# Kernel tuning notes

Hardware: AMD Instinct MI355X
Metric: run time of the kernel (lower is better)

The kernel has to match this reference:

```python
import jax, jax.numpy as jnp
import numpy as np

N = 50000
E = 800000
IN_C, C1, C2 = 256, 128, 64
BN_EPS = 1e-5


def setup_inputs() -> dict:
    key = jax.random.key(0)
    ks = jax.random.split(key, 12)
    x = jax.random.normal(ks[0], (N, IN_C), dtype=jnp.float32)
    edge_index = jax.random.randint(ks[1], (2, E), 0, N, dtype=jnp.int32)
    edge_weight = jax.random.uniform(ks[2], (E,), dtype=jnp.float32)
    W1 = jax.random.normal(ks[3], (IN_C, C1), dtype=jnp.float32) * 0.05
    b1 = jnp.zeros((C1,), dtype=jnp.float32)
    W2 = jax.random.normal(ks[4], (C1, C2), dtype=jnp.float32) * 0.05
    b2 = jnp.zeros((C2,), dtype=jnp.float32)
    g1 = jnp.ones((C1,), dtype=jnp.float32)
    be1 = jnp.zeros((C1,), dtype=jnp.float32)
    g2 = jnp.ones((C2,), dtype=jnp.float32)
    be2 = jnp.zeros((C2,), dtype=jnp.float32)
    Ws = jax.random.normal(ks[5], (IN_C, C2), dtype=jnp.float32) * 0.05
    bs = jnp.zeros((C2,), dtype=jnp.float32)
    return dict(x=x, edge_index=edge_index, edge_weight=edge_weight,
                W1=W1, b1=b1, W2=W2, b2=b2, g1=g1, be1=be1, g2=g2, be2=be2,
                Ws=Ws, bs=bs)


def _gcn_conv(h_in, row, col, ew, W, b):
    # PyG GCNConv: transform then symmetric-normalized aggregation with self-loops
    n = h_in.shape[0]
    h = h_in @ W  # [N, C]
    loop = jnp.arange(n, dtype=row.dtype)
    row_f = jnp.concatenate([row, loop])
    col_f = jnp.concatenate([col, loop])
    ew_f = jnp.concatenate([ew, jnp.ones((n,), dtype=ew.dtype)])
    deg = jax.ops.segment_sum(ew_f, col_f, num_segments=n)  # degree at targets
    dinv = jnp.where(deg > 0, jax.lax.rsqrt(deg), 0.0)
    norm = dinv[row_f] * ew_f * dinv[col_f]  # [E+N]
    out = jax.ops.segment_sum(h[row_f] * norm[:, None], col_f, num_segments=n)
    return out + b


def _batchnorm(x, gamma, beta):
    mu = jnp.mean(x, axis=0)
    var = jnp.mean(jnp.square(x - mu), axis=0)  # biased, as torch BN forward
    return (x - mu) * jax.lax.rsqrt(var + BN_EPS) * gamma + beta


def reference(x, edge_index, edge_weight, W1, b1, W2, b2, g1, be1, g2, be2, Ws, bs):
    row, col = edge_index[0], edge_index[1]
    skip = x @ Ws + bs
    x1 = _gcn_conv(x, row, col, edge_weight, W1, b1)
    x1 = jax.nn.gelu(_batchnorm(x1, g1, be1), approximate=False)
    # dropout is identity in deterministic/eval reference
    x2 = _gcn_conv(x1, row, col, edge_weight, W2, b2)
    x2 = _batchnorm(x2, g2, be2) + skip
    return x2
```

## Files before the change

kernel.cpp:

```cpp
#include <hip/hip_runtime.h>
#include <math.h>

constexpr int NN = 50000;
constexpr int EE = 800000;
constexpr int INC = 256, CC1 = 128, CC2 = 64;

typedef short bf16x8 __attribute__((ext_vector_type(8)));
typedef float f32x4 __attribute__((ext_vector_type(4)));

__device__ __forceinline__ unsigned short f2bf(float f) {
    unsigned int u = __builtin_bit_cast(unsigned int, f);
    u = (u + 0x7FFFu + ((u >> 16) & 1u)) >> 16;
    return (unsigned short)u;
}
__device__ __forceinline__ float bf2f(unsigned short u) {
    return __builtin_bit_cast(float, (unsigned int)u << 16);
}
__device__ __forceinline__ float bflo(unsigned int w) {
    return __builtin_bit_cast(float, w << 16);
}
__device__ __forceinline__ float bfhi(unsigned int w) {
    return __builtin_bit_cast(float, w & 0xFFFF0000u);
}
__device__ __forceinline__ unsigned int packbf2(float lo, float hi) {
    return (unsigned int)f2bf(lo) | ((unsigned int)f2bf(hi) << 16);
}

__global__ void __launch_bounds__(256) gemm1_rank_kernel(
        const float* __restrict__ A, const float* __restrict__ B1, const float* __restrict__ B2,
        unsigned short* __restrict__ C1, unsigned short* __restrict__ C2,
        const int* __restrict__ col, const float* __restrict__ ew,
        unsigned long long* __restrict__ packed, int* __restrict__ rank, int gemm_blocks) {
    constexpr int K = INC, N1 = CC1, N2 = CC2, NT = N1 + N2;
    constexpr int NG = 64, KC = K / 8, PITCH = K + 8;
    __shared__ unsigned short Blds[NG * PITCH];

    if ((int)blockIdx.x >= gemm_blocks) {
        int e = (blockIdx.x - gemm_blocks) * 256 + threadIdx.x;
        if (e < EE) {
            int c = col[e];
            unsigned int fx = __float2uint_rn(ew[e] * 16777216.0f);
            unsigned long long old =
                atomicAdd(&packed[c], (1ULL << 32) | (unsigned long long)fx);
            rank[e] = (int)(old >> 32);
        }
        return;
    }

    const int tid = threadIdx.x;
    const int wave = tid >> 6, lane = tid & 63;
    const int quad = lane >> 4, nIdx = lane & 15;
    const int row0 = blockIdx.x * 64 + wave * 16;
    const int arow = row0 + nIdx;
    const int arow_c = (arow < NN) ? arow : (NN - 1);

    bf16x8 afrag[K / 32];
    {
        const float* ap = A + (long long)arow_c * K + quad * 8;
#pragma unroll
        for (int s = 0; s < K / 32; s++) {
            float4 lo = *(const float4*)(ap + s * 32);
            float4 hi = *(const float4*)(ap + s * 32 + 4);
            bf16x8 f;
            f[0] = (short)f2bf(lo.x); f[1] = (short)f2bf(lo.y);
            f[2] = (short)f2bf(lo.z); f[3] = (short)f2bf(lo.w);
            f[4] = (short)f2bf(hi.x); f[5] = (short)f2bf(hi.y);
            f[6] = (short)f2bf(hi.z); f[7] = (short)f2bf(hi.w);
            afrag[s] = f;
        }
    }

    for (int g0 = 0; g0 < NT; g0 += NG) {
        if (g0) __syncthreads();
        {
            int n = tid & 63;
            int gcol = g0 + n;
            const float* Bp = B1; int Nw = N1; int bcol = gcol;
            if (gcol >= N1) { Bp = B2; Nw = N2; bcol = gcol - N1; }
            for (int kc = tid >> 6; kc < KC; kc += 4) {
                int k0 = kc * 8;
                bf16x8 v;
#pragma unroll
                for (int j = 0; j < 8; j++)
                    v[j] = (short)f2bf(Bp[(long long)(k0 + j) * Nw + bcol]);
                *(bf16x8*)(&Blds[n * PITCH + k0]) = v;
            }
        }
        __syncthreads();
#pragma unroll
        for (int t = 0; t < NG / 16; t++) {
            const unsigned short* bp = &Blds[(t * 16 + nIdx) * PITCH + quad * 8];
            f32x4 acc = {0.0f, 0.0f, 0.0f, 0.0f};
#pragma unroll
            for (int s = 0; s < K / 32; s++) {
                bf16x8 bf = *(const bf16x8*)(bp + s * 32);
                acc = __builtin_amdgcn_mfma_f32_16x16x32_bf16(afrag[s], bf, acc, 0, 0, 0);
            }
            int ocol = g0 + t * 16 + nIdx;
#pragma unroll
            for (int r = 0; r < 4; r++) {
                int orow = row0 + quad * 4 + r;
                if (orow < NN) {
                    if (ocol < N1)
                        C1[(long long)orow * N1 + ocol] = f2bf(acc[r]);
                    else
                        C2[(long long)orow * N2 + (ocol - N1)] = f2bf(acc[r]);
                }
            }
        }
    }
}


__global__ void alloc_kernel(const unsigned long long* __restrict__ packed,
                             float* __restrict__ dinv, int* __restrict__ start,
                             int* __restrict__ count, int* __restrict__ cursor, int n) {
    int i = blockIdx.x * 256 + threadIdx.x;
    if (i < n) {
        unsigned long long p = packed[i];
        int cnt = (int)(p >> 32);
        float deg = 1.0f + (float)(unsigned int)(p & 0xFFFFFFFFu) * (1.0f / 16777216.0f);
        dinv[i] = rsqrtf(deg);
        count[i] = cnt;
        start[i] = atomicAdd(cursor, cnt);
    }
}

__global__ void fill_kernel(const int* __restrict__ row, const int* __restrict__ col,
                            const float* __restrict__ ew, const float* __restrict__ dinv,
                            const int* __restrict__ rank, const int* __restrict__ start,
                            int2* __restrict__ pairs, int e_cnt) {
    int e = blockIdx.x * 256 + threadIdx.x;
    if (e < e_cnt) {
        int r = row[e], c = col[e];
        float nv = dinv[r] * ew[e] * dinv[c];
        int pos = start[c] + rank[e];
        pairs[pos] = make_int2(r, __float_as_int(nv));
    }
}

__global__ void __launch_bounds__(256) gemm2_kernel(
        const unsigned short* __restrict__ A, const float* __restrict__ B,
        unsigned short* __restrict__ C,
        const float* __restrict__ sum, const float* __restrict__ sumsq,
        const float* __restrict__ gamma, const float* __restrict__ beta, int n_rows) {
    constexpr int K = CC1, N = CC2;
    constexpr int KC = K / 8, PITCH = K + 8;
    __shared__ unsigned short Blds[N * PITCH];
    __shared__ float scL[K], shL[K];

    const int tid = threadIdx.x;
    if (tid < K) {
        float inv_n = 1.0f / (float)n_rows;
        float mu = sum[tid] * inv_n;
        float var = fmaxf(sumsq[tid] * inv_n - mu * mu, 0.0f);
        float sc = gamma[tid] * rsqrtf(var + 1e-5f);
        scL[tid] = sc; shL[tid] = beta[tid] - mu * sc;
    }
    {
        int n = tid & 63;
        for (int kc = tid >> 6; kc < KC; kc += 4) {
            int k0 = kc * 8;
            bf16x8 v;
#pragma unroll
            for (int j = 0; j < 8; j++)
                v[j] = (short)f2bf(B[(long long)(k0 + j) * N + n]);
            *(bf16x8*)(&Blds[n * PITCH + k0]) = v;
        }
    }
    __syncthreads();

    const int wave = tid >> 6, lane = tid & 63;
    const int quad = lane >> 4, nIdx = lane & 15;
    const int row0 = blockIdx.x * 64 + wave * 16;
    const int arow = row0 + nIdx;
    const int arow_c = (arow < n_rows) ? arow : (n_rows - 1);

    bf16x8 afrag[K / 32];
    {
        const unsigned short* ap = A + (long long)arow_c * K + quad * 8;
#pragma unroll
        for (int s = 0; s < K / 32; s++) {
            bf16x8 raw = *(const bf16x8*)(ap + s * 32);
            int kb = s * 32 + quad * 8;
            bf16x8 f;
#pragma unroll
            for (int j = 0; j < 8; j++) {
                float u = bf2f((unsigned short)raw[j]) * scL[kb + j] + shL[kb + j];
                float v = u * 0.5f * (1.0f + erff(u * 0.70710678f));
                f[j] = (short)f2bf(v);
            }
            afrag[s] = f;
        }
    }
#pragma unroll
    for (int t = 0; t < N / 16; t++) {
        const unsigned short* bp = &Blds[(t * 16 + nIdx) * PITCH + quad * 8];
        f32x4 acc = {0.0f, 0.0f, 0.0f, 0.0f};
#pragma unroll
        for (int s = 0; s < K / 32; s++) {
            bf16x8 bf = *(const bf16x8*)(bp + s * 32);
            acc = __builtin_amdgcn_mfma_f32_16x16x32_bf16(afrag[s], bf, acc, 0, 0, 0);
        }
        int ocol = t * 16 + nIdx;
#pragma unroll
        for (int r = 0; r < 4; r++) {
            int orow = row0 + quad * 4 + r;
            if (orow < n_rows)
                C[(long long)orow * N + ocol] = f2bf(acc[r]);
        }
    }
}

template<int C>
__global__ void gather_agg(const unsigned short* __restrict__ h, const float* __restrict__ dinv,
                           const float* __restrict__ b, const int2* __restrict__ pairs,
                           const int* __restrict__ start, const int* __restrict__ count,
                           unsigned short* __restrict__ outb, int n) {
    constexpr int TPN = C / 8;
    int gid = blockIdx.x * 256 + threadIdx.x;
    int node = gid / TPN;
    int part = gid - node * TPN;
    if (node >= n) return;
    int c8 = part * 8;
    float d = dinv[node];
    float d2 = d * d;
    uint4 hv = *(const uint4*)(h + (long long)node * C + c8);
    float a0 = bflo(hv.x) * d2 + b[c8 + 0];
    float a1 = bfhi(hv.x) * d2 + b[c8 + 1];
    float a2 = bflo(hv.y) * d2 + b[c8 + 2];
    float a3 = bfhi(hv.y) * d2 + b[c8 + 3];
    float a4 = bflo(hv.z) * d2 + b[c8 + 4];
    float a5 = bfhi(hv.z) * d2 + b[c8 + 5];
    float a6 = bflo(hv.w) * d2 + b[c8 + 6];
    float a7 = bfhi(hv.w) * d2 + b[c8 + 7];
    const int2* pp = pairs + start[node];
    int m = count[node];
    int j = 0;
    for (; j + 8 <= m; j += 8) {
        int2 p[8];
#pragma unroll
        for (int i = 0; i < 8; i++) p[i] = pp[j + i];
        uint4 v[8];
#pragma unroll
        for (int i = 0; i < 8; i++)
            v[i] = *(const uint4*)(h + (long long)p[i].x * C + c8);
#pragma unroll
        for (int i = 0; i < 8; i++) {
            float w = __int_as_float(p[i].y);
            a0 += bflo(v[i].x) * w; a1 += bfhi(v[i].x) * w;
            a2 += bflo(v[i].y) * w; a3 += bfhi(v[i].y) * w;
            a4 += bflo(v[i].z) * w; a5 += bfhi(v[i].z) * w;
            a6 += bflo(v[i].w) * w; a7 += bfhi(v[i].w) * w;
        }
    }
    for (; j < m; j++) {
        int2 p = pp[j];
        float w = __int_as_float(p.y);
        uint4 v = *(const uint4*)(h + (long long)p.x * C + c8);
        a0 += bflo(v.x) * w; a1 += bfhi(v.x) * w;
        a2 += bflo(v.y) * w; a3 += bfhi(v.y) * w;
        a4 += bflo(v.z) * w; a5 += bfhi(v.z) * w;
        a6 += bflo(v.w) * w; a7 += bfhi(v.w) * w;
    }
    uint4 o;
    o.x = packbf2(a0, a1); o.y = packbf2(a2, a3);
    o.z = packbf2(a4, a5); o.w = packbf2(a6, a7);
    *(uint4*)(outb + (long long)node * C + c8) = o;
}

template<int C>
__global__ void bnstats_bf16(const unsigned short* __restrict__ x, float* __restrict__ sum,
                             float* __restrict__ sumsq, int n) {
    constexpr int PR = C / 2;
    constexpr int RG = 256 / PR;
    constexpr int ROWS = 256;
    const int cp = threadIdx.x % PR;
    const int rg = threadIdx.x / PR;
    const int base = blockIdx.x * ROWS;
    const unsigned int* xu = (const unsigned int*)x;
    float s0 = 0, ss0 = 0, s1 = 0, ss1 = 0;
    for (int r = rg; r < ROWS; r += RG) {
        int nn = base + r;
        if (nn < n) {
            unsigned int v = xu[(long long)nn * PR + cp];
            float lo = bflo(v), hi = bfhi(v);
            s0 += lo; ss0 += lo * lo; s1 += hi; ss1 += hi * hi;
        }
    }
    __shared__ float red[4][256];
    red[0][threadIdx.x] = s0; red[1][threadIdx.x] = ss0;
    red[2][threadIdx.x] = s1; red[3][threadIdx.x] = ss1;
    __syncthreads();
    if (rg == 0) {
#pragma unroll
        for (int g = 1; g < RG; g++) {
            s0 += red[0][g * PR + cp]; ss0 += red[1][g * PR + cp];
            s1 += red[2][g * PR + cp]; ss1 += red[3][g * PR + cp];
        }
        atomicAdd(&sum[2 * cp], s0);     atomicAdd(&sumsq[2 * cp], ss0);
        atomicAdd(&sum[2 * cp + 1], s1); atomicAdd(&sumsq[2 * cp + 1], ss1);
    }
}

__global__ void final_kernel(const unsigned short* __restrict__ agg2b,
                             const unsigned short* __restrict__ skipb,
                             const float* __restrict__ sum, const float* __restrict__ sumsq,
                             const float* __restrict__ gamma, const float* __restrict__ beta,
                             const float* __restrict__ bs, float* __restrict__ out, int n) {
    __shared__ float sc[CC2], sh[CC2];
    if (threadIdx.x < CC2) {
        float inv_n = 1.0f / (float)n;
        float mu = sum[threadIdx.x] * inv_n;
        float var = fmaxf(sumsq[threadIdx.x] * inv_n - mu * mu, 0.0f);
        float s = gamma[threadIdx.x] * rsqrtf(var + 1e-5f);
        sc[threadIdx.x] = s;
        sh[threadIdx.x] = beta[threadIdx.x] - mu * s + bs[threadIdx.x];
    }
    __syncthreads();
    int i2 = blockIdx.x * 256 + threadIdx.x;
    if (i2 >= n * (CC2 / 2)) return;
    unsigned int av = ((const unsigned int*)agg2b)[i2];
    unsigned int sv = ((const unsigned int*)skipb)[i2];
    int c2 = (i2 % (CC2 / 2)) * 2;
    float2 o;
    o.x = bflo(av) * sc[c2] + sh[c2] + bflo(sv);
    o.y = bfhi(av) * sc[c2 + 1] + sh[c2 + 1] + bfhi(sv);
    *(float2*)(out + 2 * (long long)i2) = o;
}


extern "C" void kernel_launch(void* const* d_in, const int* in_sizes, int n_in,
                              void* d_out, int out_size, void* d_ws, size_t ws_size,
                              hipStream_t stream) {
    const float* x   = (const float*)d_in[0];
    const int*   ei  = (const int*)d_in[1];
    const float* ew  = (const float*)d_in[2];
    const float* W1  = (const float*)d_in[3];
    const float* b1  = (const float*)d_in[4];
    const float* W2  = (const float*)d_in[5];
    const float* b2  = (const float*)d_in[6];
    const float* g1  = (const float*)d_in[7];
    const float* be1 = (const float*)d_in[8];
    const float* g2  = (const float*)d_in[9];
    const float* be2 = (const float*)d_in[10];
    const float* Ws  = (const float*)d_in[11];
    const float* bs  = (const float*)d_in[12];
    float* out = (float*)d_out;

    const int* row = ei;
    const int* col = ei + EE;

    char* wp = (char*)d_ws;
    float* stats = (float*)wp;
    float* sum1   = stats;
    float* sumsq1 = stats + 128;
    float* sum2   = stats + 256;
    float* sumsq2 = stats + 320;
    int*   cursor = (int*)(wp + 4096);
    unsigned long long* packed = (unsigned long long*)(wp + 4112);
    char* p2 = wp + 4112 + (size_t)NN * 8;
    int*   rank   = (int*)p2;             p2 += (size_t)EE * 4;
    int*   startp = (int*)p2;             p2 += (size_t)NN * 4;
    int*   countp = (int*)p2;             p2 += (size_t)NN * 4;
    float* dinv   = (float*)p2;           p2 += (size_t)NN * 4;
    int2*  pairs  = (int2*)p2;            p2 += (size_t)EE * 8;
    unsigned short* h1b   = (unsigned short*)p2; p2 += (size_t)NN * CC1 * 2;
    unsigned short* h2b   = (unsigned short*)p2; p2 += (size_t)NN * CC2 * 2;
    unsigned short* agg1b = (unsigned short*)p2; p2 += (size_t)NN * CC1 * 2;
    unsigned short* agg2b = (unsigned short*)p2; p2 += (size_t)NN * CC2 * 2;
    unsigned short* skipb = (unsigned short*)p2; p2 += (size_t)NN * CC2 * 2;

    const int nb_N = (NN + 255) / 256;
    const int nb_E = (EE + 255) / 256;
    const int nb_G = (NN + 63) / 64;

    hipMemsetAsync(wp, 0, 4112 + (size_t)NN * 8, stream);

    gemm1_rank_kernel<<<nb_G + nb_E, 256, 0, stream>>>(
        x, W1, Ws, h1b, skipb, col, ew, packed, rank, nb_G);

    alloc_kernel<<<nb_N, 256, 0, stream>>>(packed, dinv, startp, countp, cursor, NN);
    fill_kernel<<<nb_E, 256, 0, stream>>>(row, col, ew, dinv, rank, startp, pairs, EE);

    gather_agg<CC1><<<(NN * (CC1 / 8) + 255) / 256, 256, 0, stream>>>(
        h1b, dinv, b1, pairs, startp, countp, agg1b, NN);
    bnstats_bf16<CC1><<<(NN + 255) / 256, 256, 0, stream>>>(agg1b, sum1, sumsq1, NN);

    gemm2_kernel<<<nb_G, 256, 0, stream>>>(agg1b, W2, h2b, sum1, sumsq1, g1, be1, NN);
    gather_agg<CC2><<<(NN * (CC2 / 8) + 255) / 256, 256, 0, stream>>>(
        h2b, dinv, b2, pairs, startp, countp, agg2b, NN);
    bnstats_bf16<CC2><<<(NN + 255) / 256, 256, 0, stream>>>(agg2b, sum2, sumsq2, NN);

    final_kernel<<<(NN * (CC2 / 2) + 255) / 256, 256, 0, stream>>>(
        agg2b, skipb, sum2, sumsq2, g2, be2, bs, out, NN);

    (void)in_sizes; (void)n_in; (void)out_size; (void)ws_size;
}
```

Measured before the change: 317.6 us.

## Fuse all GCN stages into one persistent cooperative kernel with grid syncs

Replaces the memset and the chain of separate kernel launches with a single cooperative persistent kernel. Stages are separated by grid.sync and use grid-stride loops. BN statistics for layer 1 are computed inside the gather stage through block reductions plus atomics, which removes a separate stats pass over agg1. This removes launch overhead and some memory re-reads, at the cost of grid-wide barriers, an occupancy-limited grid, and a GEMM1 that no longer overlaps with the rank atomics.

Result: slower. 755.3 us (+137.8%).

```diff
diff --git a/kernel.cpp b/kernel.cpp
--- a/kernel.cpp
+++ b/kernel.cpp
@@ -1,9 +1,19 @@
 #include <hip/hip_runtime.h>
+#include <hip/hip_cooperative_groups.h>
 #include <math.h>
+
+namespace cg = cooperative_groups;
 
 constexpr int NN = 50000;
 constexpr int EE = 800000;
 constexpr int INC = 256, CC1 = 128, CC2 = 64;
+
+constexpr int T1    = (NN + 63) / 64;
+constexpr int CE    = EE / 256;
+constexpr int CNODE = (NN + 255) / 256;
+constexpr int J1    = NN * (CC1 / 8) / 256;
+constexpr int J2    = (NN * (CC2 / 8) + 255) / 256;
+constexpr int F2    = NN * (CC2 / 2) / 256;
 
 typedef short bf16x8 __attribute__((ext_vector_type(8)));
 typedef float f32x4 __attribute__((ext_vector_type(4)));
@@ -26,374 +36,443 @@
     return (unsigned int)f2bf(lo) | ((unsigned int)f2bf(hi) << 16);
 }
 
-__global__ void __launch_bounds__(256) gemm1_rank_kernel(
-        const float* __restrict__ A, const float* __restrict__ B1, const float* __restrict__ B2,
-        unsigned short* __restrict__ C1, unsigned short* __restrict__ C2,
-        const int* __restrict__ col, const float* __restrict__ ew,
-        unsigned long long* __restrict__ packed, int* __restrict__ rank, int gemm_blocks) {
-    constexpr int K = INC, N1 = CC1, N2 = CC2, NT = N1 + N2;
-    constexpr int NG = 64, KC = K / 8, PITCH = K + 8;
-    __shared__ unsigned short Blds[NG * PITCH];
-
-    if ((int)blockIdx.x >= gemm_blocks) {
-        int e = (blockIdx.x - gemm_blocks) * 256 + threadIdx.x;
-        if (e < EE) {
-            int c = col[e];
-            unsigned int fx = __float2uint_rn(ew[e] * 16777216.0f);
-            unsigned long long old =
-                atomicAdd(&packed[c], (1ULL << 32) | (unsigned long long)fx);
-            rank[e] = (int)(old >> 32);
-        }
-        return;
-    }
-
+struct Params {
+    const float *x, *ew, *W1, *b1, *W2, *b2, *g1, *be1, *g2, *be2, *Ws, *bs;
+    const int *row, *col;
+    float* out;
+    float* stats;
+    int* cursor;
+    unsigned long long* packed;
+    int* rank;
+    int* startp;
+    int* countp;
+    float* dinv;
+    int2* pairs;
+    unsigned short *h1b, *h2b, *agg1b, *agg2b, *skipb;
+};
+
+union SharedU {
+    unsigned short b1[64 * (INC + 8)];
+    struct {
+        unsigned short b2[64 * (CC1 + 8)];
+        float sc[CC1], sh[CC1];
+    } g2;
+    float red[2048];
+    struct { float sc[CC2], sh[CC2]; } fin;
+};
+
+__global__ void __launch_bounds__(256, 4) mega_kernel(Params P) {
+    cg::grid_group grid = cg::this_grid();
     const int tid = threadIdx.x;
+    const int bid = blockIdx.x;
+    const int G = gridDim.x;
     const int wave = tid >> 6, lane = tid & 63;
     const int quad = lane >> 4, nIdx = lane & 15;
-    const int row0 = blockIdx.x * 64 + wave * 16;
-    const int arow = row0 + nIdx;
-    const int arow_c = (arow < NN) ? arow : (NN - 1);
-
-    bf16x8 afrag[K / 32];
+
+    __shared__ SharedU sh;
+
+    for (int c = bid; c < CNODE; c += G) {
+        int i = c * 256 + tid;
+        if (i < NN) P.packed[i] = 0ULL;
+    }
+    if (bid == 0) {
+        for (int i = tid; i < 384; i += 256) P.stats[i] = 0.0f;
+        if (tid == 0) *P.cursor = 0;
+    }
+    grid.sync();
+
     {
-        const float* ap = A + (long long)arow_c * K + quad * 8;
-#pragma unroll
-        for (int s = 0; s < K / 32; s++) {
-            float4 lo = *(const float4*)(ap + s * 32);
-            float4 hi = *(const float4*)(ap + s * 32 + 4);
-            bf16x8 f;
-            f[0] = (short)f2bf(lo.x); f[1] = (short)f2bf(lo.y);
-            f[2] = (short)f2bf(lo.z); f[3] = (short)f2bf(lo.w);
-            f[4] = (short)f2bf(hi.x); f[5] = (short)f2bf(hi.y);
-            f[6] = (short)f2bf(hi.z); f[7] = (short)f2bf(hi.w);
-            afrag[s] = f;
-        }
-    }
-
-    for (int g0 = 0; g0 < NT; g0 += NG) {
-        if (g0) __syncthreads();
+        constexpr int K = INC, N1 = CC1, N2 = CC2, NT = N1 + N2;
+        constexpr int KC = K / 8, PITCH = K + 8;
+        for (int t = bid; t < T1; t += G) {
+            const int row0 = t * 64 + wave * 16;
+            const int arow = row0 + nIdx;
+            const int arow_c = (arow < NN) ? arow : (NN - 1);
+            bf16x8 afrag[K / 32];
+            {
+                const float* ap = P.x + (long long)arow_c * K + quad * 8;
+#pragma unroll
+                for (int s = 0; s < K / 32; s++) {
+                    float4 lo = *(const float4*)(ap + s * 32);
+                    float4 hi = *(const float4*)(ap + s * 32 + 4);
+                    bf16x8 f;
+                    f[0] = (short)f2bf(lo.x); f[1] = (short)f2bf(lo.y);
+                    f[2] = (short)f2bf(lo.z); f[3] = (short)f2bf(lo.w);
+                    f[4] = (short)f2bf(hi.x); f[5] = (short)f2bf(hi.y);
+                    f[6] = (short)f2bf(hi.z); f[7] = (short)f2bf(hi.w);
+                    afrag[s] = f;
+                }
+            }
+            for (int g0 = 0; g0 < NT; g0 += 64) {
+                __syncthreads();
+                {
+                    int n = tid & 63;
+                    int gcol = g0 + n;
+                    const float* Bp = P.W1; int Nw = N1; int bcol = gcol;
+                    if (gcol >= N1) { Bp = P.Ws; Nw = N2; bcol = gcol - N1; }
+                    for (int kc = tid >> 6; kc < KC; kc += 4) {
+                        int k0 = kc * 8;
+                        bf16x8 v;
+#pragma unroll
+                        for (int j = 0; j < 8; j++)
+                            v[j] = (short)f2bf(Bp[(long long)(k0 + j) * Nw + bcol]);
+                        *(bf16x8*)(&sh.b1[n * PITCH + k0]) = v;
+                    }
+                }
+                __syncthreads();
+#pragma unroll
+                for (int t4 = 0; t4 < 4; t4++) {
+                    const unsigned short* bp = &sh.b1[(t4 * 16 + nIdx) * PITCH + quad * 8];
+                    f32x4 acc = {0.0f, 0.0f, 0.0f, 0.0f};
+#pragma unroll
+                    for (int s = 0; s < K / 32; s++) {
+                        bf16x8 bf = *(const bf16x8*)(bp + s * 32);
+                        acc = __builtin_amdgcn_mfma_f32_16x16x32_bf16(afrag[s], bf, acc, 0, 0, 0);
+                    }
+                    int ocol = g0 + t4 * 16 + nIdx;
+#pragma unroll
+                    for (int r = 0; r < 4; r++) {
+                        int orow = row0 + quad * 4 + r;
+                        if (orow < NN) {
+                            if (ocol < N1)
+                                P.h1b[(long long)orow * N1 + ocol] = f2bf(acc[r]);
+                            else
+                                P.skipb[(long long)orow * N2 + (ocol - N1)] = f2bf(acc[r]);
+                        }
+                    }
+                }
+            }
+        }
+        for (int c = bid; c < CE; c += G) {
+            int e = c * 256 + tid;
+            int cc = P.col[e];
+            unsigned int fx = __float2uint_rn(P.ew[e] * 16777216.0f);
+            unsigned long long old =
+                atomicAdd(&P.packed[cc], (1ULL << 32) | (unsigned long long)fx);
+            P.rank[e] = (int)(old >> 32);
+        }
+    }
+    grid.sync();
+
+    for (int c = bid; c < CNODE; c += G) {
+        int i = c * 256 + tid;
+        if (i < NN) {
+            unsigned long long p = P.packed[i];
+            int cnt = (int)(p >> 32);
+            float deg = 1.0f + (float)(unsigned int)(p & 0xFFFFFFFFu) * (1.0f / 16777216.0f);
+            P.dinv[i] = rsqrtf(deg);
+            P.countp[i] = cnt;
+            P.startp[i] = atomicAdd(P.cursor, cnt);
+        }
+    }
+    grid.sync();
+
+    for (int c = bid; c < CE; c += G) {
+        int e = c * 256 + tid;
+        int r = P.row[e], cc = P.col[e];
+        float nv = P.dinv[r] * P.ew[e] * P.dinv[cc];
+        P.pairs[P.startp[cc] + P.rank[e]] = make_int2(r, __float_as_int(nv));
+    }
+    grid.sync();
+
+    {
+        const int part = tid & 15;
+        const int c8 = part * 8;
+        float s[8] = {0,0,0,0,0,0,0,0}, ssq[8] = {0,0,0,0,0,0,0,0};
+        for (int j = bid; j < J1; j += G) {
+            int node = (j * 256 + tid) >> 4;
+            float d = P.dinv[node];
+            float d2 = d * d;
+            uint4 hv = *(const uint4*)(P.h1b + (long long)node * CC1 + c8);
+            float a0 = bflo(hv.x) * d2 + P.b1[c8 + 0];
+            float a1 = bfhi(hv.x) * d2 + P.b1[c8 + 1];
+            float a2 = bflo(hv.y) * d2 + P.b1[c8 + 2];
+            float a3 = bfhi(hv.y) * d2 + P.b1[c8 + 3];
+            float a4 = bflo(hv.z) * d2 + P.b1[c8 + 4];
+            float a5 = bfhi(hv.z) * d2 + P.b1[c8 + 5];
+            float a6 = bflo(hv.w) * d2 + P.b1[c8 + 6];
+            float a7 = bfhi(hv.w) * d2 + P.b1[c8 + 7];
+            const int2* pp = P.pairs + P.startp[node];
+            int m = P.countp[node];
+            int jj = 0;
+            for (; jj + 8 <= m; jj += 8) {
+                int2 p[8];
+#pragma unroll
+                for (int i = 0; i < 8; i++) p[i] = pp[jj + i];
+                uint4 v[8];
+#pragma unroll
+                for (int i = 0; i < 8; i++)
+                    v[i] = *(const uint4*)(P.h1b + (long long)p[i].x * CC1 + c8);
+#pragma unroll
+                for (int i = 0; i < 8; i++) {
+                    float w = __int_as_float(p[i].y);
+                    a0 += bflo(v[i].x) * w; a1 += bfhi(v[i].x) * w;
+                    a2 += bflo(v[i].y) * w; a3 += bfhi(v[i].y) * w;
+                    a4 += bflo(v[i].z) * w; a5 += bfhi(v[i].z) * w;
+                    a6 += bflo(v[i].w) * w; a7 += bfhi(v[i].w) * w;
+                }
+            }
+            for (; jj < m; jj++) {
+                int2 p = pp[jj];
+                float w = __int_as_float(p.y);
+                uint4 v = *(const uint4*)(P.h1b + (long long)p.x * CC1 + c8);
+                a0 += bflo(v.x) * w; a1 += bfhi(v.x) * w;
+                a2 += bflo(v.y) * w; a3 += bfhi(v.y) * w;
+                a4 += bflo(v.z) * w; a5 += bfhi(v.z) * w;
+                a6 += bflo(v.w) * w; a7 += bfhi(v.w) * w;
+            }
+            uint4 o;
+            o.x = packbf2(a0, a1); o.y = packbf2(a2, a3);
+            o.z = packbf2(a4, a5); o.w = packbf2(a6, a7);
+            *(uint4*)(P.agg1b + (long long)node * CC1 + c8) = o;
+            s[0] += a0; ssq[0] += a0 * a0; s[1] += a1; ssq[1] += a1 * a1;
+            s[2] += a2; ssq[2] += a2 * a2; s[3] += a3; ssq[3] += a3 * a3;
+            s[4] += a4; ssq[4] += a4 * a4; s[5] += a5; ssq[5] += a5 * a5;
+            s[6] += a6; ssq[6] += a6 * a6; s[7] += a7; ssq[7] += a7 * a7;
+        }
+        __syncthreads();
+#pragma unroll
+        for (int k = 0; k < 8; k++) sh.red[tid * 8 + k] = s[k];
+        __syncthreads();
+        if (tid < CC1) {
+            int p = tid >> 3, k = tid & 7;
+            float acc = 0.0f;
+#pragma unroll
+            for (int g = 0; g < 16; g++) acc += sh.red[(g * 16 + p) * 8 + k];
+            atomicAdd(&P.stats[p * 8 + k], acc);
+        }
+        __syncthreads();
+#pragma unroll
+        for (int k = 0; k < 8; k++) sh.red[tid * 8 + k] = ssq[k];
+        __syncthreads();
+        if (tid < CC1) {
+            int p = tid >> 3, k = tid & 7;
+            float acc = 0.0f;
+#pragma unroll
+            for (int g = 0; g < 16; g++) acc += sh.red[(g * 16 + p) * 8 + k];
+            atomicAdd(&P.stats[128 + p * 8 + k], acc);
+        }
+    }
+    grid.sync();
+
+    {
+        constexpr int K = CC1, N = CC2;
+        constexpr int KC = K / 8, PITCH = K + 8;
+        __syncthreads();
+        if (tid < K) {
+            float inv_n = 1.0f / (float)NN;
+            float mu = P.stats[tid] * inv_n;
+            float var = fmaxf(P.stats[128 + tid] * inv_n - mu * mu, 0.0f);
+            float sc = P.g1[tid] * rsqrtf(var + 1e-5f);
+            sh.g2.sc[tid] = sc;
+            sh.g2.sh[tid] = P.be1[tid] - mu * sc;
+        }
         {
             int n = tid & 63;
-            int gcol = g0 + n;
-            const float* Bp = B1; int Nw = N1; int bcol = gcol;
-            if (gcol >= N1) { Bp = B2; Nw = N2; bcol = gcol - N1; }
             for (int kc = tid >> 6; kc < KC; kc += 4) {
                 int k0 = kc * 8;
                 bf16x8 v;
 #pragma unroll
                 for (int j = 0; j < 8; j++)
-                    v[j] = (short)f2bf(Bp[(long long)(k0 + j) * Nw + bcol]);
-                *(bf16x8*)(&Blds[n * PITCH + k0]) = v;
-            }
-        }
-        __syncthreads();
-#pragma unroll
-        for (int t = 0; t < NG / 16; t++) {
-            const unsigned short* bp = &Blds[(t * 16 + nIdx) * PITCH + quad * 8];
-            f32x4 acc = {0.0f, 0.0f, 0.0f, 0.0f};
+                    v[j] = (short)f2bf(P.W2[(long long)(k0 + j) * N + n]);
+                *(bf16x8*)(&sh.g2.b2[n * PITCH + k0]) = v;
+            }
+        }
+        __syncthreads();
+        for (int t = bid; t < T1; t += G) {
+            const int row0 = t * 64 + wave * 16;
+            const int arow = row0 + nIdx;
+            const int arow_c = (arow < NN) ? arow : (NN - 1);
+            bf16x8 afrag[K / 32];
+            const unsigned short* ap = P.agg1b + (long long)arow_c * K + quad * 8;
 #pragma unroll
             for (int s = 0; s < K / 32; s++) {
-                bf16x8 bf = *(const bf16x8*)(bp + s * 32);
-                acc = __builtin_amdgcn_mfma_f32_16x16x32_bf16(afrag[s], bf, acc, 0, 0, 0);
-            }
-            int ocol = g0 + t * 16 + nIdx;
-#pragma unroll
-            for (int r = 0; r < 4; r++) {
-                int orow = row0 + quad * 4 + r;
-                if (orow < NN) {
-                    if (ocol < N1)
-                        C1[(long long)orow * N1 + ocol] = f2bf(acc[r]);
-                    else
-                        C2[(long long)orow * N2 + (ocol - N1)] = f2bf(acc[r]);
-                }
-            }
-        }
-    }
-}
-
-
-__global__ void alloc_kernel(const unsigned long long* __restrict__ packed,
-                             float* __restrict__ dinv, int* __restrict__ start,
-                             int* __restrict__ count, int* __restrict__ cursor, int n) {
-    int i = blockIdx.x * 256 + threadIdx.x;
-    if (i < n) {
-        unsigned long long p = packed[i];
-        int cnt = (int)(p >> 32);
-        float deg = 1.0f + (float)(unsigned int)(p & 0xFFFFFFFFu) * (1.0f / 16777216.0f);
-        dinv[i] = rsqrtf(deg);
-        count[i] = cnt;
-        start[i] = atomicAdd(cursor, cnt);
-    }
-}
-
-__global__ void fill_kernel(const int* __restrict__ row, const int* __restrict__ col,
-                            const float* __restrict__ ew, const float* __restrict__ dinv,
-                            const int* __restrict__ rank, const int* __restrict__ start,
-                            int2* __restrict__ pairs, int e_cnt) {
-    int e = blockIdx.x * 256 + threadIdx.x;
-    if (e < e_cnt) {
-        int r = row[e], c = col[e];
-        float nv = dinv[r] * ew[e] * dinv[c];
-        int pos = start[c] + rank[e];
-        pairs[pos] = make_int2(r, __float_as_int(nv));
-    }
-}
-
-__global__ void __launch_bounds__(256) gemm2_kernel(
-        const unsigned short* __restrict__ A, const float* __restrict__ B,
-        unsigned short* __restrict__ C,
-        const float* __restrict__ sum, const float* __restrict__ sumsq,
-        const float* __restrict__ gamma, const float* __restrict__ beta, int n_rows) {
-    constexpr int K = CC1, N = CC2;
-    constexpr int KC = K / 8, PITCH = K + 8;
-    __shared__ unsigned short Blds[N * PITCH];
-    __shared__ float scL[K], shL[K];
-
-    const int tid = threadIdx.x;
-    if (tid < K) {
-        float inv_n = 1.0f / (float)n_rows;
-        float mu = sum[tid] * inv_n;
-        float var = fmaxf(sumsq[tid] * inv_n - mu * mu, 0.0f);
-        float sc = gamma[tid] * rsqrtf(var + 1e-5f);
-        scL[tid] = sc; shL[tid] = beta[tid] - mu * sc;
-    }
+                bf16x8 raw = *(const bf16x8*)(ap + s * 32);
+                int kb = s * 32 + quad * 8;
+                bf16x8 f;
+#pragma unroll
+                for (int j = 0; j < 8; j++) {
+                    float u = bf2f((unsigned short)raw[j]) * sh.g2.sc[kb + j] + sh.g2.sh[kb + j];
+                    float v = u * 0.5f * (1.0f + erff(u * 0.70710678f));
+                    f[j] = (short)f2bf(v);
+                }
+                afrag[s] = f;
+            }
+#pragma unroll
+            for (int t4 = 0; t4 < N / 16; t4++) {
+                const unsigned short* bp = &sh.g2.b2[(t4 * 16 + nIdx) * PITCH + quad * 8];
+                f32x4 acc = {0.0f, 0.0f, 0.0f, 0.0f};
+#pragma unroll
+                for (int s = 0; s < K / 32; s++) {
+                    bf16x8 bf = *(const bf16x8*)(bp + s * 32);
+                    acc = __builtin_amdgcn_mfma_f32_16x16x32_bf16(afrag[s], bf, acc, 0, 0, 0);
+                }
+                int ocol = t4 * 16 + nIdx;
+#pragma unroll
+                for (int r = 0; r < 4; r++) {
+                    int orow = row0 + quad * 4 + r;
+                    if (orow < NN)
+                        P.h2b[(long long)orow * N + ocol] = f2bf(acc[r]);
+                }
+            }
+        }
+    }
+    grid.sync();
+
     {
-        int n = tid & 63;
-        for (int kc = tid >> 6; kc < KC; kc += 4) {
-            int k0 = kc * 8;
-            bf16x8 v;
-#pragma unroll
-            for (int j = 0; j < 8; j++)
-                v[j] = (short)f2bf(B[(long long)(k0 + j) * N + n]);
-            *(bf16x8*)(&Blds[n * PITCH + k0]) = v;
-        }
-    }
-    __syncthreads();
-
-    const int wave = tid >> 6, lane = tid & 63;
-    const int quad = lane >> 4, nIdx = lane & 15;
-    const int row0 = blockIdx.x * 64 + wave * 16;
-    const int arow = row0 + nIdx;
-    const int arow_c = (arow < n_rows) ? arow : (n_rows - 1);
-
-    bf16x8 afrag[K / 32];
+        const int part = tid & 7;
+        const int c8 = part * 8;
+        float s[8] = {0,0,0,0,0,0,0,0}, ssq[8] = {0,0,0,0,0,0,0,0};
+        for (int j = bid; j < J2; j += G) {
+            int node = (j * 256 + tid) >> 3;
+            if (node < NN) {
+                float d = P.dinv[node];
+                float d2 = d * d;
+                uint4 hv = *(const uint4*)(P.h2b + (long long)node * CC2 + c8);
+                float a0 = bflo(hv.x) * d2 + P.b2[c8 + 0];
+                float a1 = bfhi(hv.x) * d2 + P.b2[c8 + 1];
+                float a2 = bflo(hv.y) * d2 + P.b2[c8 + 2];
+                float a3 = bfhi(hv.y) * d2 + P.b2[c8 + 3];
+                float a4 = bflo(hv.z) * d2 + P.b2[c8 + 4];
+                float a5 = bfhi(hv.z) * d2 + P.b2[c8 + 5];
+                float a6 = bflo(hv.w) * d2 + P.b2[c8 + 6];
+                float a7 = bfhi(hv.w) * d2 + P.b2[c8 + 7];
+                const int2* pp = P.pairs + P.startp[node];
+                int m = P.countp[node];
+                int jj = 0;
+                for (; jj + 8 <= m; jj += 8) {
+                    int2 p[8];
+#pragma unroll
+                    for (int i = 0; i < 8; i++) p[i] = pp[jj + i];
+                    uint4 v[8];
+#pragma unroll
+                    for (int i = 0; i < 8; i++)
+                        v[i] = *(const uint4*)(P.h2b + (long long)p[i].x * CC2 + c8);
+#pragma unroll
+                    for (int i = 0; i < 8; i++) {
+                        float w = __int_as_float(p[i].y);
+                        a0 += bflo(v[i].x) * w; a1 += bfhi(v[i].x) * w;
+                        a2 += bflo(v[i].y) * w; a3 += bfhi(v[i].y) * w;
+                        a4 += bflo(v[i].z) * w; a5 += bfhi(v[i].z) * w;
+                        a6 += bflo(v[i].w) * w; a7 += bfhi(v[i].w) * w;
+                    }
+                }
+                for (; jj < m; jj++) {
+                    int2 p = pp[jj];
+                    float w = __int_as_float(p.y);
+                    uint4 v = *(const uint4*)(P.h2b + (long long)p.x * CC2 + c8);
+                    a0 += bflo(v.x) * w; a1 += bfhi(v.x) * w;
+                    a2 += bflo(v.y) * w; a3 += bfhi(v.y) * w;
+                    a4 += bflo(v.z) * w; a5 += bfhi(v.z) * w;
+                    a6 += bflo(v.w) * w; a7 += bfhi(v.w) * w;
+                }
+                uint4 o;
+                o.x = packbf2(a0, a1); o.y = packbf2(a2, a3);
+                o.z = packbf2(a4, a5); o.w = packbf2(a6, a7);
+                *(uint4*)(P.agg2b + (long long)node * CC2 + c8) = o;
+                s[0] += a0; ssq[0] += a0 * a0; s[1] += a1; ssq[1] += a1 * a1;
+                s[2] += a2; ssq[2] += a2 * a2; s[3] += a3; ssq[3] += a3 * a3;
+                s[4] += a4; ssq[4] += a4 * a4; s[5] += a5; ssq[5] += a5 * a5;
+                s[6] += a6; ssq[6] += a6 * a6; s[7] += a7; ssq[7] += a7 * a7;
+            }
+        }
+        __syncthreads();
+#pragma unroll
+        for (int k = 0; k < 8; k++) sh.red[tid * 8 + k] = s[k];
+        __syncthreads();
+        if (tid < CC2) {
+            int p = tid >> 3, k = tid & 7;
+            float acc = 0.0f;
+#pragma unroll
+            for (int g = 0; g < 32; g++) acc += sh.red[(g * 8 + p) * 8 + k];
+            atomicAdd(&P.stats[256 + p * 8 + k], acc);
+        }
+        __syncthreads();
+#pragma unroll
+        for (int k = 0; k < 8; k++) sh.red[tid * 8 + k] = ssq[k];
+        __syncthreads();
+        if (tid < CC2) {
+            int p = tid >> 3, k = tid & 7;
+            float acc = 0.0f;
+#pragma unroll
+            for (int g = 0; g < 32; g++) acc += sh.red[(g * 8 + p) * 8 + k];
+            atomicAdd(&P.stats[320 + p * 8 + k], acc);
+        }
+    }
+    grid.sync();
+
     {
-        const unsigned short* ap = A + (long long)arow_c * K + quad * 8;
-#pragma unroll
-        for (int s = 0; s < K / 32; s++) {
-            bf16x8 raw = *(const bf16x8*)(ap + s * 32);
-            int kb = s * 32 + quad * 8;
-            bf16x8 f;
-#pragma unroll
-            for (int j = 0; j < 8; j++) {
-                float u = bf2f((unsigned short)raw[j]) * scL[kb + j] + shL[kb + j];
-                float v = u * 0.5f * (1.0f + erff(u * 0.70710678f));
-                f[j] = (short)f2bf(v);
-            }
-            afrag[s] = f;
-        }
-    }
-#pragma unroll
-    for (int t = 0; t < N / 16; t++) {
-        const unsigned short* bp = &Blds[(t * 16 + nIdx) * PITCH + quad * 8];
-        f32x4 acc = {0.0f, 0.0f, 0.0f, 0.0f};
-#pragma unroll
-        for (int s = 0; s < K / 32; s++) {
-            bf16x8 bf = *(const bf16x8*)(bp + s * 32);
-            acc = __builtin_amdgcn_mfma_f32_16x16x32_bf16(afrag[s], bf, acc, 0, 0, 0);
-        }
-        int ocol = t * 16 + nIdx;
-#pragma unroll
-        for (int r = 0; r < 4; r++) {
-            int orow = row0 + quad * 4 + r;
-            if (orow < n_rows)
-                C[(long long)orow * N + ocol] = f2bf(acc[r]);
-        }
-    }
-}
-
-template<int C>
-__global__ void gather_agg(const unsigned short* __restrict__ h, const float* __restrict__ dinv,
-                           const float* __restrict__ b, const int2* __restrict__ pairs,
-                           const int* __restrict__ start, const int* __restrict__ count,
-                           unsigned short* __restrict__ outb, int n) {
-    constexpr int TPN = C / 8;
-    int gid = blockIdx.x * 256 + threadIdx.x;
-    int node = gid / TPN;
-    int part = gid - node * TPN;
-    if (node >= n) return;
-    int c8 = part * 8;
-    float d = dinv[node];
-    float d2 = d * d;
-    uint4 hv = *(const uint4*)(h + (long long)node * C + c8);
-    float a0 = bflo(hv.x) * d2 + b[c8 + 0];
-    float a1 = bfhi(hv.x) * d2 + b[c8 + 1];
-    float a2 = bflo(hv.y) * d2 + b[c8 + 2];
-    float a3 = bfhi(hv.y) * d2 + b[c8 + 3];
-    float a4 = bflo(hv.z) * d2 + b[c8 + 4];
-    float a5 = bfhi(hv.z) * d2 + b[c8 + 5];
-    float a6 = bflo(hv.w) * d2 + b[c8 + 6];
-    float a7 = bfhi(hv.w) * d2 + b[c8 + 7];
-    const int2* pp = pairs + start[node];
-    int m = count[node];
-    int j = 0;
-    for (; j + 8 <= m; j += 8) {
-        int2 p[8];
-#pragma unroll
-        for (int i = 0; i < 8; i++) p[i] = pp[j + i];
-        uint4 v[8];
-#pragma unroll
-        for (int i = 0; i < 8; i++)
-            v[i] = *(const uint4*)(h + (long long)p[i].x * C + c8);
-#pragma unroll
-        for (int i = 0; i < 8; i++) {
-            float w = __int_as_float(p[i].y);
-            a0 += bflo(v[i].x) * w; a1 += bfhi(v[i].x) * w;
-            a2 += bflo(v[i].y) * w; a3 += bfhi(v[i].y) * w;
-            a4 += bflo(v[i].z) * w; a5 += bfhi(v[i].z) * w;
-            a6 += bflo(v[i].w) * w; a7 += bfhi(v[i].w) * w;
-        }
-    }
-    for (; j < m; j++) {
-        int2 p = pp[j];
-        float w = __int_as_float(p.y);
-        uint4 v = *(const uint4*)(h + (long long)p.x * C + c8);
-        a0 += bflo(v.x) * w; a1 += bfhi(v.x) * w;
-        a2 += bflo(v.y) * w; a3 += bfhi(v.y) * w;
-        a4 += bflo(v.z) * w; a5 += bfhi(v.z) * w;
-        a6 += bflo(v.w) * w; a7 += bfhi(v.w) * w;
-    }
-    uint4 o;
-    o.x = packbf2(a0, a1); o.y = packbf2(a2, a3);
-    o.z = packbf2(a4, a5); o.w = packbf2(a6, a7);
-    *(uint4*)(outb + (long long)node * C + c8) = o;
-}
-
-template<int C>
-__global__ void bnstats_bf16(const unsigned short* __restrict__ x, float* __restrict__ sum,
-                             float* __restrict__ sumsq, int n) {
-    constexpr int PR = C / 2;
-    constexpr int RG = 256 / PR;
-    constexpr int ROWS = 256;
-    const int cp = threadIdx.x % PR;
-    const int rg = threadIdx.x / PR;
-    const int base = blockIdx.x * ROWS;
-    const unsigned int* xu = (const unsigned int*)x;
-    float s0 = 0, ss0 = 0, s1 = 0, ss1 = 0;
-    for (int r = rg; r < ROWS; r += RG) {
-        int nn = base + r;
-        if (nn < n) {
-            unsigned int v = xu[(long long)nn * PR + cp];
-            float lo = bflo(v), hi = bfhi(v);
-            s0 += lo; ss0 += lo * lo; s1 += hi; ss1 += hi * hi;
-        }
-    }
-    __shared__ float red[4][256];
-    red[0][threadIdx.x] = s0; red[1][threadIdx.x] = ss0;
-    red[2][threadIdx.x] = s1; red[3][threadIdx.x] = ss1;
-    __syncthreads();
-    if (rg == 0) {
-#pragma unroll
-        for (int g = 1; g < RG; g++) {
-            s0 += red[0][g * PR + cp]; ss0 += red[1][g * PR + cp];
-            s1 += red[2][g * PR + cp]; ss1 += red[3][g * PR + cp];
-        }
-        atomicAdd(&sum[2 * cp], s0);     atomicAdd(&sumsq[2 * cp], ss0);
-        atomicAdd(&sum[2 * cp + 1], s1); atomicAdd(&sumsq[2 * cp + 1], ss1);
-    }
-}
-
-__global__ void final_kernel(const unsigned short* __restrict__ agg2b,
-                             const unsigned short* __restrict__ skipb,
-                             const float* __restrict__ sum, const float* __restrict__ sumsq,
-                             const float* __restrict__ gamma, const float* __restrict__ beta,
-                             const float* __restrict__ bs, float* __restrict__ out, int n) {
-    __shared__ float sc[CC2], sh[CC2];
-    if (threadIdx.x < CC2) {
-        float inv_n = 1.0f / (float)n;
-        float mu = sum[threadIdx.x] * inv_n;
-        float var = fmaxf(sumsq[threadIdx.x] * inv_n - mu * mu, 0.0f);
-        float s = gamma[threadIdx.x] * rsqrtf(var + 1e-5f);
-        sc[threadIdx.x] = s;
-        sh[threadIdx.x] = beta[threadIdx.x] - mu * s + bs[threadIdx.x];
-    }
-    __syncthreads();
-    int i2 = blockIdx.x * 256 + threadIdx.x;
-    if (i2 >= n * (CC2 / 2)) return;
-    unsigned int av = ((const unsigned int*)agg2b)[i2];
-    unsigned int sv = ((const unsigned int*)skipb)[i2];
-    int c2 = (i2 % (CC2 / 2)) * 2;
-    float2 o;
-    o.x = bflo(av) * sc[c2] + sh[c2] + bflo(sv);
-    o.y = bfhi(av) * sc[c2 + 1] + sh[c2 + 1] + bfhi(sv);
-    *(float2*)(out + 2 * (long long)i2) = o;
+        __syncthreads();
+        if (tid < CC2) {
+            float inv_n = 1.0f / (float)NN;
+            float mu = P.stats[256 + tid] * inv_n;
+            float var = fmaxf(P.stats[320 + tid] * inv_n - mu * mu, 0.0f);
+            float s = P.g2[tid] * rsqrtf(var + 1e-5f);
+            sh.fin.sc[tid] = s;
+            sh.fin.sh[tid] = P.be2[tid] - mu * s + P.bs[tid];
+        }
+        __syncthreads();
+        const unsigned int* aggu = (const unsigned int*)P.agg2b;
+        const unsigned int* sku = (const unsigned int*)P.skipb;
+        for (int c = bid; c < F2; c += G) {
+            int i2 = c * 256 + tid;
+            unsigned int av = aggu[i2];
+            unsigned int sv = sku[i2];
+            int c2 = (i2 & 31) * 2;
+            float2 o;
+            o.x = bflo(av) * sh.fin.sc[c2] + sh.fin.sh[c2] + bflo(sv);
+            o.y = bfhi(av) * sh.fin.sc[c2 + 1] + sh.fin.sh[c2 + 1] + bfhi(sv);
+            *(float2*)(P.out + 2 * (long long)i2) = o;
+        }
+    }
 }
 
 
 extern "C" void kernel_launch(void* const* d_in, const int* in_sizes, int n_in,
                               void* d_out, int out_size, void* d_ws, size_t ws_size,
                               hipStream_t stream) {
-    const float* x   = (const float*)d_in[0];
-    const int*   ei  = (const int*)d_in[1];
-    const float* ew  = (const float*)d_in[2];
-    const float* W1  = (const float*)d_in[3];
-    const float* b1  = (const float*)d_in[4];
-    const float* W2  = (const float*)d_in[5];
-    const float* b2  = (const float*)d_in[6];
-    const float* g1  = (const float*)d_in[7];
-    const float* be1 = (const float*)d_in[8];
-    const float* g2  = (const float*)d_in[9];
-    const float* be2 = (const float*)d_in[10];
-    const float* Ws  = (const float*)d_in[11];
-    const float* bs  = (const float*)d_in[12];
-    float* out = (float*)d_out;
-
-    const int* row = ei;
-    const int* col = ei + EE;
-
     char* wp = (char*)d_ws;
-    float* stats = (float*)wp;
-    float* sum1   = stats;
-    float* sumsq1 = stats + 128;
-    float* sum2   = stats + 256;
-    float* sumsq2 = stats + 320;
-    int*   cursor = (int*)(wp + 4096);
-    unsigned long long* packed = (unsigned long long*)(wp + 4112);
-    char* p2 = wp + 4112 + (size_t)NN * 8;
-    int*   rank   = (int*)p2;             p2 += (size_t)EE * 4;
-    int*   startp = (int*)p2;             p2 += (size_t)NN * 4;
-    int*   countp = (int*)p2;             p2 += (size_t)NN * 4;
-    float* dinv   = (float*)p2;           p2 += (size_t)NN * 4;
-    int2*  pairs  = (int2*)p2;            p2 += (size_t)EE * 8;
-    unsigned short* h1b   = (unsigned short*)p2; p2 += (size_t)NN * CC1 * 2;
-    unsigned short* h2b   = (unsigned short*)p2; p2 += (size_t)NN * CC2 * 2;
-    unsigned short* agg1b = (unsigned short*)p2; p2 += (size_t)NN * CC1 * 2;
-    unsigned short* agg2b = (unsigned short*)p2; p2 += (size_t)NN * CC2 * 2;
-    unsigned short* skipb = (unsigned short*)p2; p2 += (size_t)NN * CC2 * 2;
-
-    const int nb_N = (NN + 255) / 256;
-    const int nb_E = (EE + 255) / 256;
-    const int nb_G = (NN + 63) / 64;
-
-    hipMemsetAsync(wp, 0, 4112 + (size_t)NN * 8, stream);
-
-    gemm1_rank_kernel<<<nb_G + nb_E, 256, 0, stream>>>(
-        x, W1, Ws, h1b, skipb, col, ew, packed, rank, nb_G);
-
-    alloc_kernel<<<nb_N, 256, 0, stream>>>(packed, dinv, startp, countp, cursor, NN);
-    fill_kernel<<<nb_E, 256, 0, stream>>>(row, col, ew, dinv, rank, startp, pairs, EE);
-
-    gather_agg<CC1><<<(NN * (CC1 / 8) + 255) / 256, 256, 0, stream>>>(
-        h1b, dinv, b1, pairs, startp, countp, agg1b, NN);
-    bnstats_bf16<CC1><<<(NN + 255) / 256, 256, 0, stream>>>(agg1b, sum1, sumsq1, NN);
-
-    gemm2_kernel<<<nb_G, 256, 0, stream>>>(agg1b, W2, h2b, sum1, sumsq1, g1, be1, NN);
-    gather_agg<CC2><<<(NN * (CC2 / 8) + 255) / 256, 256, 0, stream>>>(
-        h2b, dinv, b2, pairs, startp, countp, agg2b, NN);
-    bnstats_bf16<CC2><<<(NN + 255) / 256, 256, 0, stream>>>(agg2b, sum2, sumsq2, NN);
-
-    final_kernel<<<(NN * (CC2 / 2) + 255) / 256, 256, 0, stream>>>(
-        agg2b, skipb, sum2, sumsq2, g2, be2, bs, out, NN);
+    Params p;
+    p.x   = (const float*)d_in[0];
+    p.row = (const int*)d_in[1];
+    p.col = ((const int*)d_in[1]) + EE;
+    p.ew  = (const float*)d_in[2];
+    p.W1  = (const float*)d_in[3];
+    p.b1  = (const float*)d_in[4];
+    p.W2  = (const float*)d_in[5];
+    p.b2  = (const float*)d_in[6];
+    p.g1  = (const float*)d_in[7];
+    p.be1 = (const float*)d_in[8];
+    p.g2  = (const float*)d_in[9];
+    p.be2 = (const float*)d_in[10];
+    p.Ws  = (const float*)d_in[11];
+    p.bs  = (const float*)d_in[12];
+    p.out = (float*)d_out;
+
+    p.stats  = (float*)wp;
+    p.cursor = (int*)(wp + 4096);
+    p.packed = (unsigned long long*)(wp + 4112);
+    char* q = wp + 4112 + (size_t)NN * 8;
+    p.rank   = (int*)q;               q += (size_t)EE * 4;
+    p.startp = (int*)q;               q += (size_t)NN * 4;
+    p.countp = (int*)q;               q += (size_t)NN * 4;
+    p.dinv   = (float*)q;             q += (size_t)NN * 4;
+    p.pairs  = (int2*)q;              q += (size_t)EE * 8;
+    p.h1b    = (unsigned short*)q;    q += (size_t)NN * CC1 * 2;
+    p.h2b    = (unsigned short*)q;    q += (size_t)NN * CC2 * 2;
+    p.agg1b  = (unsigned short*)q;    q += (size_t)NN * CC1 * 2;
+    p.agg2b  = (unsigned short*)q;    q += (size_t)NN * CC2 * 2;
+    p.skipb  = (unsigned short*)q;    q += (size_t)NN * CC2 * 2;
+
+    int maxb = 0;
+    hipOccupancyMaxActiveBlocksPerMultiprocessor(&maxb, mega_kernel, 256, 0);
+    if (maxb < 1) maxb = 1;
+    int G = maxb * 256;
+    if (G > 2048) G = 2048;
+
+    void* args[] = {&p};
+    hipLaunchCooperativeKernel((const void*)mega_kernel, dim3(G), dim3(256),
+                               args, 0, stream);
 
     (void)in_sizes; (void)n_in; (void)out_size; (void)ws_size;
 }
```
